# Optimization experiments

Hardware: AMD Instinct MI355X
Metric: run time of the kernel (lower is better)

The kernel has to match this reference:

```python
import jax, jax.numpy as jnp
import numpy as np

B, D, M, H, K = 2048, 512, 32768, 4, 64
HD = D // H  # head_dim = 128


def setup_inputs() -> dict:
    key = jax.random.key(0)
    ks = jax.random.split(key, 10)
    s = 1.0 / np.sqrt(D)
    return {
        "query": jax.random.normal(ks[0], (B, D), jnp.float32),
        "memory": jax.random.normal(ks[1], (M, D), jnp.float32),
        "Wq": jax.random.normal(ks[2], (D, D), jnp.float32) * s,
        "bq": jax.random.normal(ks[3], (D,), jnp.float32) * s,
        "Wk": jax.random.normal(ks[4], (D, D), jnp.float32) * s,
        "bk": jax.random.normal(ks[5], (D,), jnp.float32) * s,
        "Wv": jax.random.normal(ks[6], (D, D), jnp.float32) * s,
        "bv": jax.random.normal(ks[7], (D,), jnp.float32) * s,
        "Wo": jax.random.normal(ks[8], (D, D), jnp.float32) * s,
        "bo": jax.random.normal(ks[9], (D,), jnp.float32) * s,
        "k": K,
    }


def reference(query, memory, Wq, bq, Wk, bk, Wv, bv, Wo, bo, k):
    # Linear projections (torch nn.Linear: x @ W.T + b)
    Q = (query @ Wq.T + bq).reshape(B, H, HD)      # [B, H, hd]
    Kp = (memory @ Wk.T + bk).reshape(M, H, HD)    # [M, H, hd]
    V = (memory @ Wv.T + bv).reshape(M, H, HD)     # [M, H, hd]

    scores = jnp.einsum('bhd,mhd->bhm', Q, Kp) / jnp.sqrt(jnp.float32(HD))  # [B, H, M]

    # top-k retrieval over the memory axis
    topk_scores, topk_idx = jax.lax.top_k(scores, k)          # [B, H, k]
    weights = jax.nn.softmax(topk_scores, axis=-1)            # [B, H, k]

    # gather V per head: V_topk[b,h,n,:] = V[topk_idx[b,h,n], h, :]
    Vt = jnp.transpose(V, (1, 0, 2))                          # [H, M, hd]
    V_topk = Vt[jnp.arange(H)[None, :, None], topk_idx]       # [B, H, k, hd]

    attended = jnp.einsum('bhk,bhkd->bhd', weights, V_topk)   # [B, H, hd]
    attended = attended.reshape(B, D)
    return attended @ Wo.T + bo
```

## Files before the change

kernel.cpp:

```cpp
#include <hip/hip_runtime.h>
#include <hip/hip_bf16.h>
#include <stdint.h>

#define B_  2048
#define D_  512
#define M_  32768
#define H_  4
#define HD_ 128
#define K_  64
#define MS_ 8
#define SLICE_ (M_ / MS_)
#define CH_ 128
#define ROWS_ 32
#define T_  8

typedef __attribute__((ext_vector_type(8))) short short8;
typedef __attribute__((ext_vector_type(4))) float float4v;
typedef __attribute__((ext_vector_type(2))) float float2v;

__device__ __forceinline__ ushort f2bf_rne(float f) {
  union { float f; unsigned u; } c; c.f = f;
  unsigned r = (c.u + 0x7fffu + ((c.u >> 16) & 1u)) >> 16;
  return (ushort)r;
}
__device__ __forceinline__ float bf2f(ushort u) {
  union { unsigned u; float f; } c; c.u = ((unsigned)u) << 16;
  return c.f;
}
__device__ __forceinline__ uint32_t make_key(float s, int inv) {
  union { float f; unsigned u; } c; c.f = s;
  unsigned m = c.u ^ ((unsigned)(((int)c.u) >> 31) | 0x80000000u);
  return ((m >> 16) << 13) | (unsigned)inv;
}

__global__ __launch_bounds__(256) void gemm_nt_bias(
    const float* __restrict__ X, const float* __restrict__ W,
    const float* __restrict__ bias, float* __restrict__ C, int N,
    ushort* __restrict__ Cbf) {
  __shared__ float As[16][132];
  __shared__ float Bs[16][132];
  const int t  = threadIdx.x;
  const int tx = t & 15, ty = t >> 4;
  const int rowbase = blockIdx.x * 128;
  const int colbase = blockIdx.y * 128;
  float2v acc2[8][4];
  #pragma unroll
  for (int i = 0; i < 8; ++i)
    #pragma unroll
    for (int j = 0; j < 4; ++j) acc2[i][j] = (float2v){0.f, 0.f};

  float4 va[2], vw[2];
  auto gload = [&](int k0) {
    #pragma unroll
    for (int i = 0; i < 2; ++i) {
      int idx = t + i * 256;
      int r = idx >> 2, kq = idx & 3;
      va[i] = *(const float4*)&X[(size_t)(rowbase + r) * 512 + k0 + kq * 4];
      vw[i] = *(const float4*)&W[(size_t)(colbase + r) * 512 + k0 + kq * 4];
    }
  };
  auto sstore = [&]() {
    #pragma unroll
    for (int i = 0; i < 2; ++i) {
      int idx = t + i * 256;
      int r = idx >> 2, kq = idx & 3;
      As[kq*4+0][r] = va[i].x; As[kq*4+1][r] = va[i].y;
      As[kq*4+2][r] = va[i].z; As[kq*4+3][r] = va[i].w;
      Bs[kq*4+0][r] = vw[i].x; Bs[kq*4+1][r] = vw[i].y;
      Bs[kq*4+2][r] = vw[i].z; Bs[kq*4+3][r] = vw[i].w;
    }
  };

  gload(0);
  for (int k0 = 0; k0 < 512; k0 += 16) {
    sstore();
    __syncthreads();
    if (k0 + 16 < 512) gload(k0 + 16);
    #pragma unroll
    for (int k = 0; k < 16; ++k) {
      float a[8], b[8];
      *(float4*)&a[0] = *(const float4*)&As[k][ty*8];
      *(float4*)&a[4] = *(const float4*)&As[k][ty*8+4];
      *(float4*)&b[0] = *(const float4*)&Bs[k][tx*8];
      *(float4*)&b[4] = *(const float4*)&Bs[k][tx*8+4];
      const float2v* a2 = (const float2v*)a;
      const float2v* b2 = (const float2v*)b;
      #pragma unroll
      for (int i2 = 0; i2 < 4; ++i2) {
        #pragma unroll
        for (int j = 0; j < 4; ++j) {
          asm("v_pk_fma_f32 %0, %1, %2, %0 op_sel:[0,0,0] op_sel_hi:[0,1,1]"
              : "+v"(acc2[2*i2][j]) : "v"(a2[i2]), "v"(b2[j]));
          asm("v_pk_fma_f32 %0, %1, %2, %0 op_sel:[1,0,0] op_sel_hi:[1,1,1]"
              : "+v"(acc2[2*i2+1][j]) : "v"(a2[i2]), "v"(b2[j]));
        }
      }
    }
    __syncthreads();
  }
  const int hh = colbase >> 7;
  #pragma unroll
  for (int i = 0; i < 8; ++i) {
    size_t r = (size_t)(rowbase + ty*8 + i);
    #pragma unroll
    for (int j4 = 0; j4 < 2; ++j4) {
      int c = colbase + tx*8 + j4*4;
      float4 bv = *(const float4*)&bias[c];
      float4 o;
      o.x = acc2[i][j4*2+0][0] + bv.x;
      o.y = acc2[i][j4*2+0][1] + bv.y;
      o.z = acc2[i][j4*2+1][0] + bv.z;
      o.w = acc2[i][j4*2+1][1] + bv.w;
      *(float4*)&C[r * 512 + c] = o;
      if (Cbf) {
        ushort u[4] __attribute__((aligned(8)));
        u[0] = f2bf_rne(o.x); u[1] = f2bf_rne(o.y);
        u[2] = f2bf_rne(o.z); u[3] = f2bf_rne(o.w);
        const int dd = tx * 8 + j4 * 4;
        *(ushort4*)&Cbf[((size_t)hh * N + r) * 128 + dd] = *(ushort4*)u;
      }
    }
  }
}

__global__ __launch_bounds__(256) void gemm_nt_bias64(
    const float* __restrict__ X, const float* __restrict__ W,
    const float* __restrict__ bias, float* __restrict__ C, int N,
    ushort* __restrict__ Cbf) {
  __shared__ float As[16][68];
  __shared__ float Bs[16][132];
  const int t  = threadIdx.x;
  const int tx = t & 15, ty = t >> 4;
  const int rowbase = blockIdx.x * 64;
  const int colbase = blockIdx.y * 128;
  float acc[4][8];
  #pragma unroll
  for (int i = 0; i < 4; ++i)
    #pragma unroll
    for (int j = 0; j < 8; ++j) acc[i][j] = 0.f;

  float4 va, vw[2];
  auto gload = [&](int k0) {
    { int r = t >> 2, kq = t & 3;
      va = *(const float4*)&X[(size_t)(rowbase + r) * 512 + k0 + kq * 4]; }
    #pragma unroll
    for (int i = 0; i < 2; ++i) {
      int idx = t + i * 256;
      int r = idx >> 2, kq = idx & 3;
      vw[i] = *(const float4*)&W[(size_t)(colbase + r) * 512 + k0 + kq * 4];
    }
  };
  auto sstore = [&]() {
    { int r = t >> 2, kq = t & 3;
      As[kq*4+0][r] = va.x; As[kq*4+1][r] = va.y;
      As[kq*4+2][r] = va.z; As[kq*4+3][r] = va.w; }
    #pragma unroll
    for (int i = 0; i < 2; ++i) {
      int idx = t + i * 256;
      int r = idx >> 2, kq = idx & 3;
      Bs[kq*4+0][r] = vw[i].x; Bs[kq*4+1][r] = vw[i].y;
      Bs[kq*4+2][r] = vw[i].z; Bs[kq*4+3][r] = vw[i].w;
    }
  };

  gload(0);
  for (int k0 = 0; k0 < 512; k0 += 16) {
    sstore();
    __syncthreads();
    if (k0 + 16 < 512) gload(k0 + 16);
    #pragma unroll
    for (int k = 0; k < 16; ++k) {
      float a[4], b[8];
      *(float4*)&a[0] = *(const float4*)&As[k][ty*4];
      *(float4*)&b[0] = *(const float4*)&Bs[k][tx*8];
      *(float4*)&b[4] = *(const float4*)&Bs[k][tx*8+4];
      #pragma unroll
      for (int i = 0; i < 4; ++i)
        #pragma unroll
        for (int j = 0; j < 8; ++j)
          acc[i][j] = fmaf(a[i], b[j], acc[i][j]);
    }
    __syncthreads();
  }
  const int hh = colbase >> 7;
  #pragma unroll
  for (int i = 0; i < 4; ++i) {
    size_t r = (size_t)(rowbase + ty*4 + i);
    #pragma unroll
    for (int j4 = 0; j4 < 2; ++j4) {
      int c = colbase + tx*8 + j4*4;
      float4 bv = *(const float4*)&bias[c];
      float4 o;
      o.x = acc[i][j4*4+0] + bv.x;
      o.y = acc[i][j4*4+1] + bv.y;
      o.z = acc[i][j4*4+2] + bv.z;
      o.w = acc[i][j4*4+3] + bv.w;
      *(float4*)&C[r * 512 + c] = o;
      if (Cbf) {
        ushort u[4] __attribute__((aligned(8)));
        u[0] = f2bf_rne(o.x); u[1] = f2bf_rne(o.y);
        u[2] = f2bf_rne(o.z); u[3] = f2bf_rne(o.w);
        const int dd = tx * 8 + j4 * 4;
        *(ushort4*)&Cbf[((size_t)hh * N + r) * 128 + dd] = *(ushort4*)u;
      }
    }
  }
}

__global__ __launch_bounds__(256) void split_w(
    const float* __restrict__ W, ushort* __restrict__ W1,
    ushort* __restrict__ W2) {
  const int i = (blockIdx.x * 256 + threadIdx.x) * 4;
  float4 v = *(const float4*)&W[i];
  float x[4] = {v.x, v.y, v.z, v.w};
  ushort u1[4] __attribute__((aligned(8)));
  ushort u2[4] __attribute__((aligned(8)));
  #pragma unroll
  for (int j = 0; j < 4; ++j) {
    u1[j] = f2bf_rne(x[j]);
    u2[j] = f2bf_rne(x[j] - bf2f(u1[j]));
  }
  *(ushort4*)&W1[i] = *(ushort4*)u1;
  *(ushort4*)&W2[i] = *(ushort4*)u2;
}

__global__ __launch_bounds__(256, 4) void gemm_split_nt(
    const float* __restrict__ X, const ushort* __restrict__ W1,
    const ushort* __restrict__ W2, const float* __restrict__ bias,
    float* __restrict__ C, int N) {
  const int t = threadIdx.x, w = t >> 6, lane = t & 63;
  const int l15 = lane & 15, l4 = lane >> 4;
  const int nb = blockIdx.x * 128 + w * 32;
  const int ob = blockIdx.y * 128;
  const short* w1s = (const short*)W1;
  const short* w2s = (const short*)W2;

  float4v acc[2][8];
  #pragma unroll
  for (int nt = 0; nt < 2; ++nt)
    #pragma unroll
    for (int ot = 0; ot < 8; ++ot) acc[nt][ot] = (float4v){0.f, 0.f, 0.f, 0.f};

  for (int ks = 0; ks < 16; ++ks) {
    short8 x1[2], x2[2];
    #pragma unroll
    for (int nt = 0; nt < 2; ++nt) {
      const float* xp = X + (size_t)(nb + nt * 16 + l15) * 512 + ks * 32 + l4 * 8;
      float xv[8];
      *(float4*)&xv[0] = *(const float4*)xp;
      *(float4*)&xv[4] = *(const float4*)(xp + 4);
      #pragma unroll
      for (int j = 0; j < 8; ++j) {
        ushort hi = f2bf_rne(xv[j]);
        ((ushort*)&x1[nt])[j] = hi;
        ((ushort*)&x2[nt])[j] = f2bf_rne(xv[j] - bf2f(hi));
      }
    }
    #pragma unroll
    for (int ot = 0; ot < 8; ++ot) {
      const size_t wo = (size_t)(ob + ot * 16 + l15) * 512 + ks * 32 + l4 * 8;
      short8 wf1 = *(const short8*)(w1s + wo);
      short8 wf2 = *(const short8*)(w2s + wo);
      #pragma unroll
      for (int nt = 0; nt < 2; ++nt) {
        acc[nt][ot] = __builtin_amdgcn_mfma_f32_16x16x32_bf16(wf1, x1[nt], acc[nt][ot], 0, 0, 0);
        acc[nt][ot] = __builtin_amdgcn_mfma_f32_16x16x32_bf16(wf2, x1[nt], acc[nt][ot], 0, 0, 0);
        acc[nt][ot] = __builtin_amdgcn_mfma_f32_16x16x32_bf16(wf1, x2[nt], acc[nt][ot], 0, 0, 0);
      }
    }
  }

  #pragma unroll
  for (int nt = 0; nt < 2; ++nt) {
    const size_t row = (size_t)(nb + nt * 16 + l15);
    #pragma unroll
    for (int ot = 0; ot < 8; ++ot) {
      const int col = ob + ot * 16 + l4 * 4;
      float4 bv = *(const float4*)&bias[col];
      float4 o;
      o.x = acc[nt][ot][0] + bv.x;
      o.y = acc[nt][ot][1] + bv.y;
      o.z = acc[nt][ot][2] + bv.z;
      o.w = acc[nt][ot][3] + bv.w;
      *(float4*)&C[row * 512 + col] = o;
    }
  }
}

__global__ __launch_bounds__(256, 4) void scores_topk_ll(
    const ushort* __restrict__ Qbf, const ushort* __restrict__ Kbf,
    uint32_t* __restrict__ tkp) {
  const int t = threadIdx.x, w = t >> 6, lane = t & 63;
  const int l   = blockIdx.x;
  const int xcd = l & 7;
  const int i2  = l >> 3;
  const int s   = xcd + 8 * (i2 >> 6);
  const int h   = s >> 3, z = s & 7;
  const int rowbase = (i2 & 63) * ROWS_;
  const int mbase = z * SLICE_;
  const int l15 = lane & 15, l4 = lane >> 4;

  short8 qf0[4], qf1[4];
  {
    const short* Q0 = (const short*)Qbf +
        ((size_t)h * B_ + rowbase + l15) * 128 + l4 * 8;
    const short* Q1 = (const short*)Qbf +
        ((size_t)h * B_ + rowbase + 16 + l15) * 128 + l4 * 8;
    #pragma unroll
    for (int ks = 0; ks < 4; ++ks) {
      qf0[ks] = *(const short8*)(Q0 + ks * 32);
      qf1[ks] = *(const short8*)(Q1 + ks * 32);
    }
  }

  const short* Kh = (const short*)Kbf + (size_t)h * M_ * 128;

  uint32_t kt0[T_], kt1[T_];
  #pragma unroll
  for (int j = 0; j < T_; ++j) { kt0[j] = 0u; kt1[j] = 0u; }

  auto ins = [&](uint32_t c, uint32_t* kt) {
    uint32_t prev = kt[0];
    kt[0] = (kt[0] >= c) ? kt[0] : c;
    #pragma unroll
    for (int i = 1; i < T_; ++i) {
      uint32_t cur = kt[i];
      uint32_t nv;
      asm("v_med3_u32 %0, %1, %2, %3" : "=v"(nv) : "v"(prev), "v"(cur), "v"(c));
      kt[i] = nv;
      prev = cur;
    }
  };

  for (int ch = 0; ch < SLICE_ / CH_; ++ch) {
    const int mb = mbase + ch * CH_;
    short8 buf[8];
    #pragma unroll
    for (int tt = 0; tt < 2; ++tt) {
      const short* Ka = Kh + (size_t)(mb + 32 * w + 16 * tt + l15) * 128 + l4 * 8;
      #pragma unroll
      for (int ks = 0; ks < 4; ++ks)
        buf[tt * 4 + ks] = *(const short8*)(Ka + ks * 32);
    }
    #pragma unroll
    for (int tt = 0; tt < 2; ++tt) {
      const int inv0 = SLICE_ - 1 - (ch * CH_ + 32 * w + 16 * tt + 4 * l4);
      float4v a0 = {0.f, 0.f, 0.f, 0.f};
      float4v a1 = {0.f, 0.f, 0.f, 0.f};
      #pragma unroll
      for (int ks = 0; ks < 4; ++ks) {
        a0 = __builtin_amdgcn_mfma_f32_16x16x32_bf16(buf[tt * 4 + ks], qf0[ks], a0, 0, 0, 0);
        a1 = __builtin_amdgcn_mfma_f32_16x16x32_bf16(buf[tt * 4 + ks], qf1[ks], a1, 0, 0, 0);
      }
      #pragma unroll
      for (int reg = 0; reg < 4; ++reg) ins(make_key(a0[reg], inv0 - reg), kt0);
      #pragma unroll
      for (int reg = 0; reg < 4; ++reg) ins(make_key(a1[reg], inv0 - reg), kt1);
    }
  }

  const int id = w * 4 + l4;
  const size_t base0 =
      ((((size_t)(rowbase + l15)) * H_ + h) * MS_ + z) * (16 * T_) + (size_t)id * T_;
  const size_t base1 =
      ((((size_t)(rowbase + 16 + l15)) * H_ + h) * MS_ + z) * (16 * T_) + (size_t)id * T_;
  #pragma unroll
  for (int j = 0; j < T_; ++j) {
    tkp[base0 + j] = kt0[j];
    tkp[base1 + j] = kt1[j];
  }
}

__global__ __launch_bounds__(256) void topk_select(
    const uint32_t* __restrict__ tkp, int* __restrict__ tki) {
  __shared__ unsigned h1[256];
  __shared__ unsigned h2[256];
  __shared__ unsigned bstar, cstar, nabove;
  __shared__ int ocnt;
  __shared__ int outi[256];
  const int t = threadIdx.x;
  const int bh = blockIdx.x;
  const uint32_t* src = tkp + (size_t)bh * (MS_ * 16 * T_);
  uint32_t k[4];
  #pragma unroll
  for (int j = 0; j < 4; ++j) k[j] = src[j * 256 + t];
  h1[t] = 0; h2[t] = 0;
  if (t == 0) ocnt = 0;
  __syncthreads();
  #pragma unroll
  for (int j = 0; j < 4; ++j) atomicAdd(&h1[k[j] >> 24], 1u);
  __syncthreads();
  unsigned v = h1[t];
  for (int d = 1; d < 256; d <<= 1) {
    unsigned o = (t + d < 256) ? h1[t + d] : 0u;
    __syncthreads();
    v += o; h1[t] = v;
    __syncthreads();
  }
  if (h1[t] >= 64u && (t == 255 || h1[t + 1] < 64u)) {
    bstar = (unsigned)t; nabove = (t == 255) ? 0u : h1[t + 1];
  }
  __syncthreads();
  const unsigned bs = bstar, na = nabove;
  #pragma unroll
  for (int j = 0; j < 4; ++j)
    if ((k[j] >> 24) == bs) atomicAdd(&h2[(k[j] >> 16) & 0xFFu], 1u);
  __syncthreads();
  v = h2[t];
  for (int d = 1; d < 256; d <<= 1) {
    unsigned o = (t + d < 256) ? h2[t + d] : 0u;
    __syncthreads();
    v += o; h2[t] = v;
    __syncthreads();
  }
  if (na + h2[t] >= 64u && (t == 255 || na + h2[t + 1] < 64u)) cstar = (unsigned)t;
  __syncthreads();
  const uint32_t theta = ((((bs << 8) | cstar) << 16)) - 65536u;
  #pragma unroll
  for (int j = 0; j < 4; ++j) {
    if (k[j] >= theta) {
      int p = atomicAdd(&ocnt, 1);
      if (p < 256) {
        const int pos = j * 256 + t;
        const int z = pos >> 7;
        const int ci = (SLICE_ - 1) - (int)(k[j] & 0xFFFu);
        outi[p] = (z << 12) | ci;
      }
    }
  }
  __syncthreads();
  int n = ocnt; if (n > 256) n = 256;
  if (t >= n) outi[t] = -(t + 1);
  __syncthreads();
  tki[(size_t)bh * 256 + t] = outi[t];
}

__global__ __launch_bounds__(256) void rescore_attend(
    const float* __restrict__ Qp, const float* __restrict__ Kp,
    const float* __restrict__ Vp, const int* __restrict__ tki,
    float* __restrict__ att) {
  __shared__ float q_[128];
  __shared__ float s_[256];
  __shared__ int   i_[256];
  __shared__ float wsm[64];
  __shared__ int   widx[64];
  const int bh = blockIdx.x, b = bh >> 2, h = bh & 3;
  const int t = threadIdx.x, w = t >> 6, lane = t & 63;
  const float SCALE = 0.08838834764831843f;

  if (t < 32) *(float4*)&q_[t * 4] = *(const float4*)&Qp[(size_t)b * 512 + h * 128 + t * 4];
  i_[t] = tki[(size_t)bh * 256 + t];
  __syncthreads();

  const int o = lane >> 3, il = lane & 7;
  #pragma unroll 2
  for (int p = 0; p < 8; ++p) {
    const int j = w * 64 + p * 8 + o;
    const int idx = i_[j];
    const float* kr = Kp + (size_t)(idx < 0 ? 0 : idx) * 512 + h * 128;
    float part = 0.f;
    #pragma unroll
    for (int u = 0; u < 4; ++u) {
      const int f = il + u * 8;
      float4 kv = *(const float4*)&kr[f * 4];
      float4 qv = *(const float4*)&q_[f * 4];
      part += kv.x * qv.x + kv.y * qv.y + kv.z * qv.z + kv.w * qv.w;
    }
    part += __shfl_xor(part, 1);
    part += __shfl_xor(part, 2);
    part += __shfl_xor(part, 4);
    if (il == 0) s_[j] = (idx < 0) ? -3.0e38f : part * SCALE;
  }
  __syncthreads();

  for (int k = 2; k <= 256; k <<= 1) {
    for (int j = k >> 1; j > 0; j >>= 1) {
      if (t < 128) {
        const int i = ((t & ~(j - 1)) << 1) | (t & (j - 1));
        const int p2 = i | j;
        const bool dir = ((i & k) == 0);
        float sa = s_[i], sb = s_[p2];
        int   ia = i_[i], ib = i_[p2];
        const bool inorder = (sa > sb) || (sa == sb && ia <= ib);
        if (inorder != dir) { s_[i] = sb; s_[p2] = sa; i_[i] = ib; i_[p2] = ia; }
      }
      __syncthreads();
    }
  }

  if (t < 64) {
    float sv = s_[t];
    float mx = sv;
    #pragma unroll
    for (int off = 32; off; off >>= 1) mx = fmaxf(mx, __shfl_xor(mx, off));
    float e = expf(sv - mx);
    float zz = e;
    #pragma unroll
    for (int off = 32; off; off >>= 1) zz += __shfl_xor(zz, off);
    wsm[t] = e / zz;
    widx[t] = i_[t];
  }
  __syncthreads();

  if (t < 128) {
    float a = 0.f;
    #pragma unroll 4
    for (int k2 = 0; k2 < 64; ++k2)
      a = fmaf(wsm[k2], Vp[(size_t)widx[k2] * 512 + h * 128 + t], a);
    att[(size_t)b * 512 + h * 128 + t] = a;
  }
}

extern "C" void kernel_launch(void* const* d_in, const int* in_sizes, int n_in,
                              void* d_out, int out_size, void* d_ws, size_t ws_size,
                              hipStream_t stream) {
  const float* query  = (const float*)d_in[0];
  const float* memory = (const float*)d_in[1];
  const float* Wq = (const float*)d_in[2];
  const float* bq = (const float*)d_in[3];
  const float* Wk = (const float*)d_in[4];
  const float* bk = (const float*)d_in[5];
  const float* Wv = (const float*)d_in[6];
  const float* bv = (const float*)d_in[7];
  const float* Wo = (const float*)d_in[8];
  const float* bo = (const float*)d_in[9];
  float* out = (float*)d_out;

  float*  Qp  = (float*)d_ws;
  float*  Kp  = Qp + (size_t)B_ * D_;
  float*  Vp  = Kp + (size_t)M_ * D_;
  int*    tki = (int*)(Vp + (size_t)M_ * D_);
  ushort* Qbf = (ushort*)(tki + (size_t)B_ * H_ * 256);
  ushort* Kbf = Qbf + (size_t)H_ * B_ * 128;
  uint32_t* tkp = (uint32_t*)Vp;
  float*  att = (float*)Kbf;
  ushort* w1v = Kbf + (size_t)2 * 1024 * 1024;
  ushort* w2v = w1v + (size_t)D_ * D_;

  gemm_nt_bias64<<<dim3(B_ / 64, 4), 256, 0, stream>>>(query, Wq, bq, Qp, B_, Qbf);
  gemm_nt_bias<<<dim3(M_ / 128, 4), 256, 0, stream>>>(memory, Wk, bk, Kp, M_, Kbf);

  scores_topk_ll<<<dim3(2048), 256, 0, stream>>>(Qbf, Kbf, tkp);
  topk_select<<<dim3(B_ * H_), 256, 0, stream>>>(tkp, tki);

  split_w<<<dim3(256), 256, 0, stream>>>(Wv, w1v, w2v);
  gemm_split_nt<<<dim3(M_ / 128, 4), 256, 0, stream>>>(memory, w1v, w2v, bv, Vp, M_);

  rescore_attend<<<dim3(B_ * H_), 256, 0, stream>>>(Qp, Kp, Vp, tki, att);

  gemm_nt_bias64<<<dim3(B_ / 64, 4), 256, 0, stream>>>(att, Wo, bo, out, B_, nullptr);
}
```

Baseline: 826.8 us.

## Double-buffer K loads with inline asm prefetch in scores/top-k kernel

```diff
diff --git a/kernel.cpp b/kernel.cpp
--- a/kernel.cpp
+++ b/kernel.cpp
@@ -287,7 +287,7 @@
   }
 }
 
-__global__ __launch_bounds__(256, 4) void scores_topk_ll(
+__global__ __launch_bounds__(256, 3) void scores_topk_ll(
     const ushort* __restrict__ Qbf, const ushort* __restrict__ Kbf,
     uint32_t* __restrict__ tkp) {
   const int t = threadIdx.x, w = t >> 6, lane = t & 63;
@@ -332,16 +332,24 @@
     }
   };
 
-  for (int ch = 0; ch < SLICE_ / CH_; ++ch) {
-    const int mb = mbase + ch * CH_;
-    short8 buf[8];
-    #pragma unroll
-    for (int tt = 0; tt < 2; ++tt) {
-      const short* Ka = Kh + (size_t)(mb + 32 * w + 16 * tt + l15) * 128 + l4 * 8;
-      #pragma unroll
-      for (int ks = 0; ks < 4; ++ks)
-        buf[tt * 4 + ks] = *(const short8*)(Ka + ks * 32);
-    }
+  uint64_t adr[8];
+  #pragma unroll
+  for (int tt = 0; tt < 2; ++tt)
+    #pragma unroll
+    for (int ks = 0; ks < 4; ++ks)
+      adr[tt * 4 + ks] = (uint64_t)(Kh +
+          (size_t)(mbase + 32 * w + 16 * tt + l15) * 128 + ks * 32 + l4 * 8);
+
+  short8 bufA[8], bufB[8];
+  auto issue = [&](short8 (&buf)[8]) {
+    #pragma unroll
+    for (int i = 0; i < 8; ++i) {
+      asm volatile("global_load_dwordx4 %0, %1, off"
+                   : "=&v"(buf[i]) : "v"(adr[i]));
+      adr[i] += (uint64_t)(CH_ * 128 * 2);
+    }
+  };
+  auto compute = [&](int ch, short8 (&buf)[8]) {
     #pragma unroll
     for (int tt = 0; tt < 2; ++tt) {
       const int inv0 = SLICE_ - 1 - (ch * CH_ + 32 * w + 16 * tt + 4 * l4);
@@ -357,6 +365,23 @@
       #pragma unroll
       for (int reg = 0; reg < 4; ++reg) ins(make_key(a1[reg], inv0 - reg), kt1);
     }
+  };
+
+  const int NCH = SLICE_ / CH_;
+  issue(bufA);
+  for (int ch = 0; ch < NCH; ch += 2) {
+    issue(bufB);
+    asm volatile("s_waitcnt vmcnt(8)" ::: "memory");
+    __builtin_amdgcn_sched_barrier(0);
+    compute(ch, bufA);
+    if (ch + 2 < NCH) {
+      issue(bufA);
+      asm volatile("s_waitcnt vmcnt(8)" ::: "memory");
+    } else {
+      asm volatile("s_waitcnt vmcnt(0)" ::: "memory");
+    }
+    __builtin_amdgcn_sched_barrier(0);
+    compute(ch + 1, bufB);
   }
 
   const int id = w * 4 + l4;
```

New measurement: 799.5 us. -3.3%, faster.
